# Performance work log

Measured on AMD Instinct MI355X. Metric: run time of the kernel, lower is better.

## Reference

```python
import jax, jax.numpy as jnp
import numpy as np

D_MODEL, H, D_FF = 1024, 16, 4096
D_K = D_MODEL // H
EPS = 1e-6
NEG = -1e9


def _layer_norm(x, alpha, bias):
    # torch LayerNormalization: scalar alpha/bias, unbiased std (ddof=1), eps added to std
    n = x.shape[-1]
    mu = jnp.mean(x, axis=-1, keepdims=True)
    var = jnp.sum((x - mu) ** 2, axis=-1, keepdims=True) / (n - 1)
    std = jnp.sqrt(var)
    return alpha * (x - mu) / (std + EPS) + bias


def _linear(x, w, b):
    # torch nn.Linear: y = x @ W^T + b, W: [out, in]
    return jnp.einsum('bsd,od->bso', x, w) + b


def setup_inputs() -> dict:
    key = jax.random.key(0)
    ks = jax.random.split(key, 12)
    d, dff = D_MODEL, D_FF
    s_d = 1.0 / np.sqrt(d)
    s_ff = 1.0 / np.sqrt(dff)
    inp = {
        'x': jax.random.normal(ks[0], (2, 2048, d), dtype=jnp.float32),
        'mask': jnp.ones((2, 1, 1, 2048), dtype=jnp.int32),
        'wq': jax.random.uniform(ks[1], (d, d), jnp.float32, -s_d, s_d),
        'bq': jnp.zeros((d,), jnp.float32),
        'wk': jax.random.uniform(ks[2], (d, d), jnp.float32, -s_d, s_d),
        'bk': jnp.zeros((d,), jnp.float32),
        'wv': jax.random.uniform(ks[3], (d, d), jnp.float32, -s_d, s_d),
        'bv': jnp.zeros((d,), jnp.float32),
        'wo': jax.random.uniform(ks[4], (d, d), jnp.float32, -s_d, s_d),
        'bo': jnp.zeros((d,), jnp.float32),
        'w1': jax.random.uniform(ks[5], (dff, d), jnp.float32, -s_d, s_d),
        'b1': jnp.zeros((dff,), jnp.float32),
        'w2': jax.random.uniform(ks[6], (d, dff), jnp.float32, -s_ff, s_ff),
        'b2': jnp.zeros((d,), jnp.float32),
        'ln1_a': jnp.ones((1,), jnp.float32),
        'ln1_b': jnp.zeros((1,), jnp.float32),
        'ln2_a': jnp.ones((1,), jnp.float32),
        'ln2_b': jnp.zeros((1,), jnp.float32),
    }
    return inp


def reference(x, mask, wq, bq, wk, bk, wv, bv, wo, bo, w1, b1, w2, b2,
              ln1_a, ln1_b, ln2_a, ln2_b):
    b, s, d = x.shape

    # --- residual 1: pre-norm self-attention (dropout is identity in eval) ---
    xn = _layer_norm(x, ln1_a, ln1_b)
    q = _linear(xn, wq, bq).reshape(b, s, H, D_K).transpose(0, 2, 1, 3)  # [b,h,s,dk]
    k = _linear(xn, wk, bk).reshape(b, s, H, D_K).transpose(0, 2, 1, 3)
    v = _linear(xn, wv, bv).reshape(b, s, H, D_K).transpose(0, 2, 1, 3)
    scores = jnp.einsum('bhqd,bhkd->bhqk', q, k) / jnp.sqrt(jnp.float32(D_K))
    scores = jnp.where(mask == 0, NEG, scores)
    p = jax.nn.softmax(scores, axis=-1)
    attn = jnp.einsum('bhqk,bhkd->bhqd', p, v)
    attn = attn.transpose(0, 2, 1, 3).reshape(b, s, d)
    x = x + _linear(attn, wo, bo)

    # --- residual 2: pre-norm feed-forward ---
    xn = _layer_norm(x, ln2_a, ln2_b)
    h = jax.nn.relu(_linear(xn, w1, b1))
    x = x + _linear(h, w2, b2)
    return x
```

## Files before the change

### kernel.cpp

```cpp
#include <hip/hip_runtime.h>
#include <hip/hip_bf16.h>
#include <stdint.h>

typedef __bf16 bf16x8 __attribute__((ext_vector_type(8)));
typedef __bf16 bf16x4 __attribute__((ext_vector_type(4)));
typedef short  s16x4  __attribute__((ext_vector_type(4)));
typedef float  f32x4  __attribute__((ext_vector_type(4)));
typedef unsigned short u16;

__device__ __forceinline__ u16 f2bf(float f) {
    return __builtin_bit_cast(u16, (__bf16)f);
}

__device__ __forceinline__ f32x4 vexp4(f32x4 a) {
    f32x4 r;
    r[0] = __expf(a[0]); r[1] = __expf(a[1]);
    r[2] = __expf(a[2]); r[3] = __expf(a[3]);
    return r;
}

__device__ __forceinline__ f32x4 mfma16(bf16x4 a, bf16x4 b, f32x4 c) {
#if __has_builtin(__builtin_amdgcn_mfma_f32_16x16x16bf16_1k)
    return __builtin_amdgcn_mfma_f32_16x16x16bf16_1k(
        __builtin_bit_cast(s16x4, a), __builtin_bit_cast(s16x4, b), c, 0, 0, 0);
#else
    f32x4 d;
    asm volatile("v_mfma_f32_16x16x16_bf16 %0, %1, %2, %3"
                 : "=v"(d) : "v"(a), "v"(b), "v"(c));
    return d;
#endif
}

__device__ __forceinline__ void stage16(const void* g, void* lds_wave_base) {
#if __has_builtin(__builtin_amdgcn_global_load_lds)
    __builtin_amdgcn_global_load_lds(
        (const __attribute__((address_space(1))) void*)g,
        (__attribute__((address_space(3))) void*)lds_wave_base, 16, 0, 0);
#else
    int lane = threadIdx.x & 63;
    *(uint4*)((char*)lds_wave_base + lane * 16) = *(const uint4*)g;
#endif
}

__device__ __forceinline__ int swz(int r) {
    return (((r) & 7) ^ (((r) >> 3) & 7)) << 4;
}
__device__ __forceinline__ int vswz(int r) {
    return (((r) & 15) ^ ((r) >> 4)) << 4;
}

__global__ void pack1_kernel(const float* __restrict__ wq, const float* __restrict__ wk,
                             const float* __restrict__ wv, const float* __restrict__ bq,
                             const float* __restrict__ bk, const float* __restrict__ bv,
                             const float* __restrict__ wo,
                             u16* __restrict__ wqkv, float* __restrict__ bqkv,
                             u16* __restrict__ wo_b) {
    const float QS = 0.125f;
    size_t i0 = (size_t)blockIdx.x * 256 + threadIdx.x;
    size_t stride = (size_t)gridDim.x * 256;
    const size_t DD = 1024u * 1024u;
    for (size_t i = i0; i < 3 * DD; i += stride) {
        float v;
        if (i < DD)          v = wq[i] * QS;
        else if (i < 2 * DD) v = wk[i - DD];
        else                 v = wv[i - 2 * DD];
        wqkv[i] = f2bf(v);
    }
    for (size_t i = i0; i < DD; i += stride) wo_b[i] = f2bf(wo[i]);
    for (size_t i = i0; i < 3072; i += stride)
        bqkv[i] = (i < 1024) ? bq[i] * QS : ((i < 2048) ? bk[i - 1024] : bv[i - 2048]);
}

__global__ void pack2_kernel(const float* __restrict__ w1, const float* __restrict__ w2,
                             u16* __restrict__ w1_b, u16* __restrict__ w2_b) {
    size_t i0 = (size_t)blockIdx.x * 256 + threadIdx.x;
    size_t stride = (size_t)gridDim.x * 256;
    const size_t DD = 1024u * 1024u;
    for (size_t i = i0; i < 4 * DD; i += stride) w1_b[i] = f2bf(w1[i]);
    for (size_t i = i0; i < 4 * DD; i += stride) w2_b[i] = f2bf(w2[i]);
}

__global__ __launch_bounds__(256)
void ln_kernel(const float* __restrict__ x, u16* __restrict__ out,
               const float* __restrict__ alpha, const float* __restrict__ beta) {
    const int row = blockIdx.x;
    const int t = threadIdx.x, lane = t & 63, w = t >> 6;
    float4 v = ((const float4*)(x + (size_t)row * 1024))[t];
    float s  = v.x + v.y + v.z + v.w;
    float ss = v.x * v.x + v.y * v.y + v.z * v.z + v.w * v.w;
#pragma unroll
    for (int d = 1; d < 64; d <<= 1) { s += __shfl_xor(s, d); ss += __shfl_xor(ss, d); }
    __shared__ float red[8];
    if (lane == 0) { red[w] = s; red[4 + w] = ss; }
    __syncthreads();
    s  = red[0] + red[1] + red[2] + red[3];
    ss = red[4] + red[5] + red[6] + red[7];
    const float mu  = s * (1.f / 1024.f);
    const float var = fmaxf((ss - 1024.f * mu * mu) * (1.f / 1023.f), 0.f);
    const float inv = alpha[0] / (sqrtf(var) + 1e-6f);
    const float bb  = beta[0];
    ushort4 o;
    o.x = f2bf((v.x - mu) * inv + bb);
    o.y = f2bf((v.y - mu) * inv + bb);
    o.z = f2bf((v.z - mu) * inv + bb);
    o.w = f2bf((v.w - mu) * inv + bb);
    ((ushort4*)(out + (size_t)row * 1024))[t] = o;
}

template <int EPI>
__global__ __launch_bounds__(256)
void gemm_bt(const u16* __restrict__ A, const u16* __restrict__ B,
             const float* __restrict__ bias, const float* __restrict__ resid,
             void* __restrict__ Cout, int M, int N, int K, int ldc) {
    __shared__ __align__(16) char As[16384];
    __shared__ __align__(16) char Bs[16384];
    const int t = threadIdx.x;
    const int lane = t & 63, wave = t >> 6;
    const int g = lane >> 4, c = lane & 15;
    const int wm = wave >> 1, wn = wave & 1;
    const int bm = blockIdx.x, bn = blockIdx.y;

    const f32x4 z4 = {0.f, 0.f, 0.f, 0.f};
    f32x4 acc[4][4];
#pragma unroll
    for (int m = 0; m < 4; ++m)
#pragma unroll
        for (int n = 0; n < 4; ++n) acc[m][n] = z4;

    const int srow = t >> 2;
    const int ak = (((t & 3) ^ ((t >> 2) & 3)) << 3);
    const u16* ga = A + (size_t)(bm * 128 + srow) * K + ak;
    const u16* gb = B + (size_t)(bn * 128 + srow) * K + ak;
    const size_t rstep = (size_t)64 * K;

    auto STAGE = [&](int k0, int buf) {
        char* la = As + buf * 8192 + wave * 1024;
        char* lb = Bs + buf * 8192 + wave * 1024;
        stage16(ga + k0,         la);
        stage16(ga + k0 + rstep, la + 4096);
        stage16(gb + k0,         lb);
        stage16(gb + k0 + rstep, lb + 4096);
    };

    STAGE(0, 0);
    asm volatile("s_waitcnt vmcnt(0)" ::: "memory");
    __syncthreads();

    int cur = 0;
    for (int k0 = 0; k0 < K; k0 += 32) {
        if (k0 + 32 < K) STAGE(k0 + 32, cur ^ 1);
        const char* Ac = As + cur * 8192;
        const char* Bc = Bs + cur * 8192;
        bf16x8 a[4], b[4];
#pragma unroll
        for (int m = 0; m < 4; ++m) {
            int r = wm * 64 + m * 16 + c;
            a[m] = *(const bf16x8*)(Ac + r * 64 + ((g * 16) ^ ((c & 3) << 4)));
        }
#pragma unroll
        for (int n = 0; n < 4; ++n) {
            int r = wn * 64 + n * 16 + c;
            b[n] = *(const bf16x8*)(Bc + r * 64 + ((g * 16) ^ ((c & 3) << 4)));
        }
        __builtin_amdgcn_s_setprio(1);
#pragma unroll
        for (int m = 0; m < 4; ++m)
#pragma unroll
            for (int n = 0; n < 4; ++n)
                acc[m][n] = __builtin_amdgcn_mfma_f32_16x16x32_bf16(a[m], b[n], acc[m][n], 0, 0, 0);
        __builtin_amdgcn_s_setprio(0);
        asm volatile("s_waitcnt vmcnt(0)" ::: "memory");
        __syncthreads();
        cur ^= 1;
    }

    const int row0 = bm * 128 + wm * 64;
    const int col0 = bn * 128 + wn * 64;
#pragma unroll
    for (int m = 0; m < 4; ++m) {
#pragma unroll
        for (int n = 0; n < 4; ++n) {
            const int cc = col0 + n * 16 + c;
            const float bv = bias[cc];
#pragma unroll
            for (int j = 0; j < 4; ++j) {
                const int rr = row0 + m * 16 + g * 4 + j;
                float v = acc[m][n][j] + bv;
                if (EPI == 1) v = v > 0.f ? v : 0.f;
                if (EPI == 2) {
                    ((float*)Cout)[(size_t)rr * ldc + cc] = resid[(size_t)rr * ldc + cc] + v;
                } else {
                    ((u16*)Cout)[(size_t)rr * ldc + cc] = f2bf(v);
                }
            }
        }
    }
}

template <int EPI>
__global__ __launch_bounds__(512)
void gemm256(const u16* __restrict__ A, const u16* __restrict__ B,
             const float* __restrict__ bias, u16* __restrict__ Cout,
             int K, int ldc, int gm) {
    extern __shared__ __align__(16) char lds[];
    char* As0 = lds;
    char* Bs0 = lds + 65536;
    const int t = threadIdx.x, lane = t & 63, wave = t >> 6;
    const int g = lane >> 4, c = lane & 15;
    const int wm = wave >> 2, wn = wave & 3;
    const int f = blockIdx.x, nb = gridDim.x;
    const int sw = (f & 7) * (nb >> 3) + (f >> 3);
    const int bm = sw % gm, bn = sw / gm;

    const f32x4 z4 = {0.f, 0.f, 0.f, 0.f};
    f32x4 acc[8][4];
#pragma unroll
    for (int mi = 0; mi < 8; ++mi)
#pragma unroll
        for (int ni = 0; ni < 4; ++ni) acc[mi][ni] = z4;

    auto STAGE = [&](const u16* G, int base_row, int k0, char* dst, int half) {
#pragma unroll
        for (int l = 0; l < 2; ++l) {
            int idx = half * 1024 + l * 512 + t;
            int row = idx >> 3, p = idx & 7;
            stage16(G + (size_t)(base_row + row) * K + k0 + ((p ^ (row & 7)) << 3),
                    dst + (half * 1024 + l * 512 + wave * 64) * 16);
        }
    };
    auto ldA = [&](int buf, int mi, int ks) -> bf16x8 {
        int r = wm * 128 + mi * 16 + c;
        return *(const bf16x8*)(As0 + buf * 32768 + r * 128 + ((((ks << 2) + g) ^ (r & 7)) << 4));
    };
    auto ldB = [&](int buf, int ni, int ks) -> bf16x8 {
        int r = wn * 64 + ni * 16 + c;
        return *(const bf16x8*)(Bs0 + buf * 32768 + r * 128 + ((((ks << 2) + g) ^ (r & 7)) << 4));
    };

    const int NT = K >> 6;
    STAGE(A, bm * 256, 0, As0, 0); STAGE(A, bm * 256, 0, As0, 1);
    STAGE(B, bn * 256, 0, Bs0, 0); STAGE(B, bn * 256, 0, Bs0, 1);
    asm volatile("s_waitcnt vmcnt(0)" ::: "memory");
    __builtin_amdgcn_s_barrier();

    int cur = 0;
    for (int kt = 0; kt < NT; ++kt) {
        const int k0n = (kt + 1) << 6;
        const bool more = kt + 1 < NT;
        bf16x8 bfr[4][2];
#pragma unroll
        for (int ni = 0; ni < 4; ++ni) {
            bfr[ni][0] = ldB(cur, ni, 0);
            bfr[ni][1] = ldB(cur, ni, 1);
        }
#pragma unroll
        for (int ph = 0; ph < 4; ++ph) {
            bf16x8 a0k0 = ldA(cur, 2 * ph, 0),     a0k1 = ldA(cur, 2 * ph, 1);
            bf16x8 a1k0 = ldA(cur, 2 * ph + 1, 0), a1k1 = ldA(cur, 2 * ph + 1, 1);
            if (more && ph == 0) {
                STAGE(A, bm * 256, k0n, As0 + (cur ^ 1) * 32768, 0);
                STAGE(A, bm * 256, k0n, As0 + (cur ^ 1) * 32768, 1);
            }
            if (more && ph == 1) {
                STAGE(B, bn * 256, k0n, Bs0 + (cur ^ 1) * 32768, 0);
                STAGE(B, bn * 256, k0n, Bs0 + (cur ^ 1) * 32768, 1);
            }
            __builtin_amdgcn_s_barrier();
            __builtin_amdgcn_s_setprio(1);
#pragma unroll
            for (int ni = 0; ni < 4; ++ni) {
                acc[2 * ph][ni]     = __builtin_amdgcn_mfma_f32_16x16x32_bf16(a0k0, bfr[ni][0], acc[2 * ph][ni], 0, 0, 0);
                acc[2 * ph][ni]     = __builtin_amdgcn_mfma_f32_16x16x32_bf16(a0k1, bfr[ni][1], acc[2 * ph][ni], 0, 0, 0);
                acc[2 * ph + 1][ni] = __builtin_amdgcn_mfma_f32_16x16x32_bf16(a1k0, bfr[ni][0], acc[2 * ph + 1][ni], 0, 0, 0);
                acc[2 * ph + 1][ni] = __builtin_amdgcn_mfma_f32_16x16x32_bf16(a1k1, bfr[ni][1], acc[2 * ph + 1][ni], 0, 0, 0);
            }
            __builtin_amdgcn_s_setprio(0);
            __builtin_amdgcn_s_barrier();
        }
        asm volatile("s_waitcnt vmcnt(0)" ::: "memory");
        __builtin_amdgcn_s_barrier();
        cur ^= 1;
    }

    const int row0 = bm * 256 + wm * 128;
    const int col0 = bn * 256 + wn * 64;
#pragma unroll
    for (int mi = 0; mi < 8; ++mi) {
#pragma unroll
        for (int ni = 0; ni < 4; ++ni) {
            const int cc = col0 + ni * 16 + c;
            const float bv = bias[cc];
#pragma unroll
            for (int j = 0; j < 4; ++j) {
                const int rr = row0 + mi * 16 + g * 4 + j;
                float v = acc[mi][ni][j] + bv;
                if (EPI == 1) v = v > 0.f ? v : 0.f;
                Cout[(size_t)rr * ldc + cc] = f2bf(v);
            }
        }
    }
}

__global__ __launch_bounds__(256)
void attn_kernel(const u16* __restrict__ qkv, const int* __restrict__ mask,
                 u16* __restrict__ attn_out) {
    __shared__ __align__(16) char Ksm[32768];
    __shared__ __align__(16) char Vsm[16384];
    const int t = threadIdx.x, lane = t & 63, w = t >> 6;
    const int g = lane >> 4, c = lane & 15;
    const int flat = blockIdx.x;
    const int xcd = flat & 7, u = flat >> 3;
    const int qt = u & 31;
    const int p = xcd * 4 + (u >> 5);
    const int h = p & 15, b = p >> 4;
    const int S = 2048, LD = 3072;
    const int NT = S / 128;

    bf16x8 qf[2];
#pragma unroll
    for (int half = 0; half < 2; ++half)
        qf[half] = *(const bf16x8*)&qkv[(size_t)(b * S + qt * 64 + w * 16 + c) * LD
                                        + h * 64 + half * 32 + g * 8];

    const f32x4 z4 = {0.f, 0.f, 0.f, 0.f};
    f32x4 accO[4];
#pragma unroll
    for (int dt = 0; dt < 4; ++dt) accO[dt] = z4;
    f32x4 lrun4 = z4;

    unsigned vr[2][8];
    const int vd0 = (t & 31) * 2;
    const int vkg[2] = {t >> 5, 8 + (t >> 5)};

    auto STAGEK = [&](int kt, char* Kd) {
#pragma unroll
        for (int it = 0; it < 4; ++it) {
            int idx = it * 256 + t;
            int k = idx >> 3, pp = idx & 7;
            int ps = pp ^ ((k & 7) ^ ((k >> 3) & 7));
            stage16(&qkv[(size_t)(b * S + kt * 128 + k) * LD + 1024 + h * 64 + ps * 8],
                    Kd + (it * 256 + w * 64) * 16);
        }
    };
    auto VLOAD = [&](int kt) {
#pragma unroll
        for (int it = 0; it < 2; ++it) {
            const u16* src = &qkv[(size_t)(b * S + kt * 128 + vkg[it] * 8) * LD + 2048 + h * 64 + vd0];
#pragma unroll
            for (int i = 0; i < 8; ++i)
                vr[it][i] = *(const unsigned*)(src + (size_t)i * LD);
        }
    };
    auto VWRITE = [&]() {
#pragma unroll
        for (int it = 0; it < 2; ++it) {
            int d0 = vd0, kg = vkg[it];
            uint4 lo, hi;
            lo.x = (vr[it][0] & 0xffffu) | (vr[it][1] << 16);
            lo.y = (vr[it][2] & 0xffffu) | (vr[it][3] << 16);
            lo.z = (vr[it][4] & 0xffffu) | (vr[it][5] << 16);
            lo.w = (vr[it][6] & 0xffffu) | (vr[it][7] << 16);
            hi.x = (vr[it][0] >> 16) | (vr[it][1] & 0xffff0000u);
            hi.y = (vr[it][2] >> 16) | (vr[it][3] & 0xffff0000u);
            hi.z = (vr[it][4] >> 16) | (vr[it][5] & 0xffff0000u);
            hi.w = (vr[it][6] >> 16) | (vr[it][7] & 0xffff0000u);
            *(uint4*)(Vsm + d0 * 256 + ((kg * 16) ^ vswz(d0)))           = lo;
            *(uint4*)(Vsm + (d0 + 1) * 256 + ((kg * 16) ^ vswz(d0 + 1))) = hi;
        }
    };

    STAGEK(0, Ksm);
    VLOAD(0);
    asm volatile("s_waitcnt vmcnt(0)" ::: "memory");
    VWRITE();
    __syncthreads();

    int cur = 0;
    for (int kt = 0; kt < NT; ++kt) {
        char* Kc = Ksm + cur * 16384;
        if (kt + 1 < NT) {
            STAGEK(kt + 1, Ksm + (cur ^ 1) * 16384);
            VLOAD(kt + 1);
        }

        f32x4 s[8];
        __builtin_amdgcn_s_setprio(1);
#pragma unroll
        for (int n = 0; n < 8; ++n) {
            int kr = n * 16 + c;
            bf16x8 k0 = *(const bf16x8*)(Kc + kr * 128 + ((g * 16) ^ swz(kr)));
            bf16x8 k1 = *(const bf16x8*)(Kc + kr * 128 + ((64 + g * 16) ^ swz(kr)));
            s[n] = __builtin_amdgcn_mfma_f32_16x16x32_bf16(k0, qf[0], z4, 0, 0, 0);
            s[n] = __builtin_amdgcn_mfma_f32_16x16x32_bf16(k1, qf[1], s[n], 0, 0, 0);
        }
        __builtin_amdgcn_s_setprio(0);
#pragma unroll
        for (int n = 0; n < 8; ++n) {
            int4 mv = *(const int4*)&mask[b * S + kt * 128 + n * 16 + g * 4];
            if (mv.x == 0) s[n][0] = -1e9f;
            if (mv.y == 0) s[n][1] = -1e9f;
            if (mv.z == 0) s[n][2] = -1e9f;
            if (mv.w == 0) s[n][3] = -1e9f;
        }
#pragma unroll
        for (int n = 0; n < 8; ++n) { s[n] = vexp4(s[n]); lrun4 += s[n]; }
        __builtin_amdgcn_s_setprio(1);
#pragma unroll
        for (int n = 0; n < 8; ++n) {
            bf16x4 p0;
#pragma unroll
            for (int j = 0; j < 4; ++j) p0[j] = (__bf16)s[n][j];
#pragma unroll
            for (int dt = 0; dt < 4; ++dt) {
                int d = dt * 16 + c;
                bf16x4 vf = *(const bf16x4*)(Vsm + d * 256 + ((n * 32 + g * 8) ^ vswz(d)));
                accO[dt] = mfma16(vf, p0, accO[dt]);
            }
        }
        __builtin_amdgcn_s_setprio(0);

        __syncthreads();
        asm volatile("s_waitcnt vmcnt(0)" ::: "memory");
        if (kt + 1 < NT) VWRITE();
        __syncthreads();
        cur ^= 1;
    }

    char* Osm = Ksm;
    {
        float l = lrun4[0] + lrun4[1] + lrun4[2] + lrun4[3];
        l += __shfl_xor(l, 16);
        l += __shfl_xor(l, 32);
        float inv = 1.f / l;
        int ql = w * 16 + c;
#pragma unroll
        for (int dt = 0; dt < 4; ++dt)
#pragma unroll
            for (int j = 0; j < 4; ++j) {
                int d = dt * 16 + g * 4 + j;
                *(u16*)(Osm + ql * 128 + ((d * 2) ^ swz(ql))) = f2bf(accO[dt][j] * inv);
            }
    }
    __syncthreads();
#pragma unroll
    for (int it = 0; it < 2; ++it) {
        int idx = it * 256 + t;
        int q = idx >> 3, pp = idx & 7;
        uint4 val = *(const uint4*)(Osm + q * 128 + ((pp * 16) ^ swz(q)));
        *(uint4*)&attn_out[(size_t)(b * S + qt * 64 + q) * 1024 + h * 64 + pp * 8] = val;
    }
}

extern "C" void kernel_launch(void* const* d_in, const int* in_sizes, int n_in,
                              void* d_out, int out_size, void* d_ws, size_t ws_size,
                              hipStream_t stream) {
    const float* x    = (const float*)d_in[0];
    const int*   mask = (const int*)d_in[1];
    const float* wq   = (const float*)d_in[2];
    const float* bq   = (const float*)d_in[3];
    const float* wk   = (const float*)d_in[4];
    const float* bk   = (const float*)d_in[5];
    const float* wv   = (const float*)d_in[6];
    const float* bv   = (const float*)d_in[7];
    const float* wo   = (const float*)d_in[8];
    const float* bo   = (const float*)d_in[9];
    const float* w1   = (const float*)d_in[10];
    const float* b1   = (const float*)d_in[11];
    const float* w2   = (const float*)d_in[12];
    const float* b2   = (const float*)d_in[13];
    const float* ln1a = (const float*)d_in[14];
    const float* ln1b = (const float*)d_in[15];
    const float* ln2a = (const float*)d_in[16];
    const float* ln2b = (const float*)d_in[17];

    const size_t MB = 1048576;
    char* ws = (char*)d_ws;
    const bool big = ws_size >= 88 * MB;

    hipFuncSetAttribute(reinterpret_cast<const void*>(gemm256<0>),
                        hipFuncAttributeMaxDynamicSharedMemorySize, 131072);
    hipFuncSetAttribute(reinterpret_cast<const void*>(gemm256<1>),
                        hipFuncAttributeMaxDynamicSharedMemorySize, 131072);

    u16 *xn, *wqkv, *wo_b, *qkvb, *attnb, *w1_b, *w2_b, *hbuf;
    float *bqkv, *x1;
    if (big) {
        xn    = (u16*)(ws + 0 * MB);
        wqkv  = (u16*)(ws + 8 * MB);
        wo_b  = (u16*)(ws + 14 * MB);
        qkvb  = (u16*)(ws + 16 * MB);
        attnb = (u16*)(ws + 40 * MB);
        x1    = (float*)(ws + 48 * MB);
        w1_b  = (u16*)(ws + 64 * MB);
        w2_b  = (u16*)(ws + 72 * MB);
        hbuf  = (u16*)(ws + 16 * MB);
        bqkv  = (float*)(ws + 80 * MB);
    } else {
        xn    = (u16*)(ws + 0 * MB);
        wqkv  = (u16*)(ws + 8 * MB);
        wo_b  = (u16*)(ws + 14 * MB);
        qkvb  = (u16*)(ws + 16 * MB);
        attnb = (u16*)(ws + 40 * MB);
        x1    = (float*)(ws + 16 * MB);
        w1_b  = (u16*)(ws + 32 * MB);
        w2_b  = (u16*)(ws + 8 * MB);
        hbuf  = (u16*)(ws + 40 * MB);
        bqkv  = (float*)(ws + 40 * MB);
    }

    pack1_kernel<<<1024, 256, 0, stream>>>(wq, wk, wv, bq, bk, bv, wo, wqkv, bqkv, wo_b);
    ln_kernel<<<4096, 256, 0, stream>>>(x, xn, ln1a, ln1b);
    gemm256<0><<<192, 512, 131072, stream>>>(xn, wqkv, bqkv, qkvb, 1024, 3072, 16);
    attn_kernel<<<1024, 256, 0, stream>>>(qkvb, mask, attnb);
    gemm_bt<2><<<dim3(32, 8), 256, 0, stream>>>(attnb, wo_b, bo, x, x1,
                                                4096, 1024, 1024, 1024);
    pack2_kernel<<<1024, 256, 0, stream>>>(w1, w2, w1_b, w2_b);
    ln_kernel<<<4096, 256, 0, stream>>>(x1, xn, ln2a, ln2b);

    if (big) {
        gemm256<1><<<256, 512, 131072, stream>>>(xn, w1_b, b1, hbuf, 1024, 4096, 16);
        gemm_bt<2><<<dim3(32, 8), 256, 0, stream>>>(hbuf, w2_b, b2, x1, (float*)d_out,
                                                    4096, 1024, 4096, 1024);
    } else {
        const int mrows = 1024;
        for (int cidx = 0; cidx < 4; ++cidx) {
            const size_t ro = (size_t)cidx * mrows;
            gemm_bt<1><<<dim3(mrows / 128, 32), 256, 0, stream>>>(
                xn + ro * 1024, w1_b, b1, nullptr, hbuf, mrows, 4096, 1024, 4096);
            gemm_bt<2><<<dim3(mrows / 128, 8), 256, 0, stream>>>(
                hbuf, w2_b, b2, x1 + ro * 1024, (float*)d_out + ro * 1024,
                mrows, 1024, 4096, 1024);
        }
    }
}
```

Measured before the change: 287.2 us.

## Fold log2e into Q scale, use exp2, 16x16x32 PV MFMA, merge weight packing

Folds log2(e) into the Q weight and bias scale so the softmax can use exp2 in place of exp. The P·V product moves from 16x16x16 MFMAs to 16x16x32 MFMAs by packing two probability fragments and two V fragments together, halving the MFMA count. When the large workspace is available, FFN weight conversion runs inside the first pack kernel with a doubled grid, removing one launch. Risks include slightly different rounding from the extra scale in bf16, and the packed V loads must match the K-ordering the MFMA expects.

```diff
diff --git a/kernel.cpp b/kernel.cpp
--- a/kernel.cpp
+++ b/kernel.cpp
@@ -12,23 +12,11 @@
     return __builtin_bit_cast(u16, (__bf16)f);
 }
 
-__device__ __forceinline__ f32x4 vexp4(f32x4 a) {
+__device__ __forceinline__ f32x4 vexp2_4(f32x4 a) {
     f32x4 r;
-    r[0] = __expf(a[0]); r[1] = __expf(a[1]);
-    r[2] = __expf(a[2]); r[3] = __expf(a[3]);
+    r[0] = exp2f(a[0]); r[1] = exp2f(a[1]);
+    r[2] = exp2f(a[2]); r[3] = exp2f(a[3]);
     return r;
-}
-
-__device__ __forceinline__ f32x4 mfma16(bf16x4 a, bf16x4 b, f32x4 c) {
-#if __has_builtin(__builtin_amdgcn_mfma_f32_16x16x16bf16_1k)
-    return __builtin_amdgcn_mfma_f32_16x16x16bf16_1k(
-        __builtin_bit_cast(s16x4, a), __builtin_bit_cast(s16x4, b), c, 0, 0, 0);
-#else
-    f32x4 d;
-    asm volatile("v_mfma_f32_16x16x16_bf16 %0, %1, %2, %3"
-                 : "=v"(d) : "v"(a), "v"(b), "v"(c));
-    return d;
-#endif
 }
 
 __device__ __forceinline__ void stage16(const void* g, void* lds_wave_base) {
@@ -52,10 +40,12 @@
 __global__ void pack1_kernel(const float* __restrict__ wq, const float* __restrict__ wk,
                              const float* __restrict__ wv, const float* __restrict__ bq,
                              const float* __restrict__ bk, const float* __restrict__ bv,
-                             const float* __restrict__ wo,
+                             const float* __restrict__ wo, const float* __restrict__ w1,
+                             const float* __restrict__ w2,
                              u16* __restrict__ wqkv, float* __restrict__ bqkv,
-                             u16* __restrict__ wo_b) {
-    const float QS = 0.125f;
+                             u16* __restrict__ wo_b, u16* __restrict__ w1_b,
+                             u16* __restrict__ w2_b, int do_ffn) {
+    const float QS = 0.125f * 1.44269504088896f;
     size_t i0 = (size_t)blockIdx.x * 256 + threadIdx.x;
     size_t stride = (size_t)gridDim.x * 256;
     const size_t DD = 1024u * 1024u;
@@ -67,6 +57,10 @@
         wqkv[i] = f2bf(v);
     }
     for (size_t i = i0; i < DD; i += stride) wo_b[i] = f2bf(wo[i]);
+    if (do_ffn) {
+        for (size_t i = i0; i < 4 * DD; i += stride) w1_b[i] = f2bf(w1[i]);
+        for (size_t i = i0; i < 4 * DD; i += stride) w2_b[i] = f2bf(w2[i]);
+    }
     for (size_t i = i0; i < 3072; i += stride)
         bqkv[i] = (i < 1024) ? bq[i] * QS : ((i < 2048) ? bk[i - 1024] : bv[i - 2048]);
 }
@@ -403,18 +397,24 @@
             if (mv.w == 0) s[n][3] = -1e9f;
         }
 #pragma unroll
-        for (int n = 0; n < 8; ++n) { s[n] = vexp4(s[n]); lrun4 += s[n]; }
+        for (int n = 0; n < 8; ++n) { s[n] = vexp2_4(s[n]); lrun4 += s[n]; }
         __builtin_amdgcn_s_setprio(1);
 #pragma unroll
-        for (int n = 0; n < 8; ++n) {
-            bf16x4 p0;
-#pragma unroll
-            for (int j = 0; j < 4; ++j) p0[j] = (__bf16)s[n][j];
+        for (int i = 0; i < 4; ++i) {
+            bf16x8 p8;
+#pragma unroll
+            for (int j = 0; j < 4; ++j) {
+                p8[j]     = (__bf16)s[2 * i][j];
+                p8[4 + j] = (__bf16)s[2 * i + 1][j];
+            }
 #pragma unroll
             for (int dt = 0; dt < 4; ++dt) {
                 int d = dt * 16 + c;
-                bf16x4 vf = *(const bf16x4*)(Vsm + d * 256 + ((n * 32 + g * 8) ^ vswz(d)));
-                accO[dt] = mfma16(vf, p0, accO[dt]);
+                uint2 vlo = *(const uint2*)(Vsm + d * 256 + ((i * 64 + g * 8) ^ vswz(d)));
+                uint2 vhi = *(const uint2*)(Vsm + d * 256 + ((i * 64 + 32 + g * 8) ^ vswz(d)));
+                uint4 vv = {vlo.x, vlo.y, vhi.x, vhi.y};
+                bf16x8 vf = __builtin_bit_cast(bf16x8, vv);
+                accO[dt] = __builtin_amdgcn_mfma_f32_16x16x32_bf16(vf, p8, accO[dt], 0, 0, 0);
             }
         }
         __builtin_amdgcn_s_setprio(0);
@@ -508,13 +508,13 @@
         bqkv  = (float*)(ws + 40 * MB);
     }
 
-    pack1_kernel<<<1024, 256, 0, stream>>>(wq, wk, wv, bq, bk, bv, wo, wqkv, bqkv, wo_b);
+    pack1_kernel<<<2048, 256, 0, stream>>>(wq, wk, wv, bq, bk, bv, wo, w1, w2,
+                                           wqkv, bqkv, wo_b, w1_b, w2_b, big ? 1 : 0);
     ln_kernel<<<4096, 256, 0, stream>>>(x, xn, ln1a, ln1b);
     gemm256<0><<<192, 512, 131072, stream>>>(xn, wqkv, bqkv, qkvb, 1024, 3072, 16);
     attn_kernel<<<1024, 256, 0, stream>>>(qkvb, mask, attnb);
     gemm_bt<2><<<dim3(32, 8), 256, 0, stream>>>(attnb, wo_b, bo, x, x1,
                                                 4096, 1024, 1024, 1024);
-    pack2_kernel<<<1024, 256, 0, stream>>>(w1, w2, w1_b, w2_b);
     ln_kernel<<<4096, 256, 0, stream>>>(x1, xn, ln2a, ln2b);
 
     if (big) {
@@ -522,6 +522,7 @@
         gemm_bt<2><<<dim3(32, 8), 256, 0, stream>>>(hbuf, w2_b, b2, x1, (float*)d_out,
                                                     4096, 1024, 4096, 1024);
     } else {
+        pack2_kernel<<<1024, 256, 0, stream>>>(w1, w2, w1_b, w2_b);
         const int mrows = 1024;
         for (int cidx = 0; cidx < 4; ++cidx) {
             const size_t ro = (size_t)cidx * mrows;
```

Measured after the change: 289.4 us. About the same (+0.8%).
